# Kernel tuning notes

Measured on AMD Instinct MI355X. Metric: run time of the kernel, lower is better.

The kernel has to match this reference:

```python
import jax, jax.numpy as jnp
import numpy as np

IN_FEATURES = 4096
OUT_FEATURES = 11008
B, S = 4, 2048


def setup_inputs() -> dict:
    key = jax.random.key(0)
    k1, k2, k3, k4 = jax.random.split(key, 4)
    x = jax.random.normal(k1, (B, S, IN_FEATURES), dtype=jnp.float32)
    # int8 quantized weights in [-127, 127]
    weight_quantized = jax.random.randint(k2, (OUT_FEATURES, IN_FEATURES), -127, 128, dtype=jnp.int8)
    # realistic per-channel scales (positive, small)
    weight_scale = jax.random.uniform(k3, (OUT_FEATURES,), dtype=jnp.float32, minval=1e-4, maxval=2e-2)
    bias = jax.random.normal(k4, (OUT_FEATURES,), dtype=jnp.float32) * 0.01
    return {"x": x, "weight_quantized": weight_quantized, "weight_scale": weight_scale, "bias": bias}


def reference(x, weight_quantized, weight_scale, bias):
    # Dequantize: W = int8.float() * scale[:, None]  (symmetric, per-channel)
    w = weight_quantized.astype(jnp.float32) * weight_scale[:, None]  # [out, in]
    # F.linear: y = x @ W^T + b
    return jnp.einsum('bsi,oi->bso', x, w) + bias
```

## Files before the change

### kernel.cpp

```cpp
#include <hip/hip_runtime.h>
#include <hip/hip_bf16.h>
#include <stdint.h>


#define M_TOTAL 8192
#define K_TOTAL 4096
#define N_TOTAL 11008
#define NT 32
#define NBM 64
#define NBN 86

typedef __attribute__((ext_vector_type(4))) int int4v;


__global__ __launch_bounds__(256) void quant_x_kernel(const float* __restrict__ x,
                                                      signed char* __restrict__ xq,
                                                      float* __restrict__ sx) {
    const int row = blockIdx.x;
    const int tid = threadIdx.x;
    const float* xr = x + (size_t)row * K_TOTAL + tid * 16;

    float4 v0 = reinterpret_cast<const float4*>(xr)[0];
    float4 v1 = reinterpret_cast<const float4*>(xr)[1];
    float4 v2 = reinterpret_cast<const float4*>(xr)[2];
    float4 v3 = reinterpret_cast<const float4*>(xr)[3];

    float m = 0.f;
    m = fmaxf(m, fmaxf(fmaxf(fabsf(v0.x), fabsf(v0.y)), fmaxf(fabsf(v0.z), fabsf(v0.w))));
    m = fmaxf(m, fmaxf(fmaxf(fabsf(v1.x), fabsf(v1.y)), fmaxf(fabsf(v1.z), fabsf(v1.w))));
    m = fmaxf(m, fmaxf(fmaxf(fabsf(v2.x), fabsf(v2.y)), fmaxf(fabsf(v2.z), fabsf(v2.w))));
    m = fmaxf(m, fmaxf(fmaxf(fabsf(v3.x), fabsf(v3.y)), fmaxf(fabsf(v3.z), fabsf(v3.w))));

    for (int d = 1; d < 64; d <<= 1) m = fmaxf(m, __shfl_xor(m, d));
    __shared__ float wm_[4];
    if ((tid & 63) == 0) wm_[tid >> 6] = m;
    __syncthreads();
    m = fmaxf(fmaxf(wm_[0], wm_[1]), fmaxf(wm_[2], wm_[3]));

    const float inv = (m > 0.f) ? (127.f / m) : 0.f;
    if (tid == 0) sx[row] = (m > 0.f) ? (m / 127.f) : 0.f;

    float tmp[16] = {v0.x,v0.y,v0.z,v0.w, v1.x,v1.y,v1.z,v1.w,
                     v2.x,v2.y,v2.z,v2.w, v3.x,v3.y,v3.z,v3.w};
    int q[16];
#pragma unroll
    for (int i = 0; i < 16; ++i) {
        int t = __float2int_rn(tmp[i] * inv);
        q[i] = t > 127 ? 127 : (t < -127 ? -127 : t);
    }
    int4v o;
#pragma unroll
    for (int w = 0; w < 4; ++w)
        o[w] = (q[w*4] & 255) | ((q[w*4+1] & 255) << 8) |
               ((q[w*4+2] & 255) << 16) | ((q[w*4+3] & 255) << 24);
    *reinterpret_cast<int4v*>(xq + (size_t)row * K_TOTAL + tid * 16) = o;
}


__global__ __launch_bounds__(256) void cvt_w_kernel(const int* __restrict__ in,
                                                    signed char* __restrict__ out, int nitems) {
    bool is8 = false;
    for (int i = 0; i < 256; ++i) {
        int v = in[i];
        if (v < -127 || v > 127) { is8 = true; break; }
    }
    int stride = gridDim.x * blockDim.x;
    if (!is8) {
        for (int i = blockIdx.x * blockDim.x + threadIdx.x; i < nitems; i += stride) {
            const int* p = in + (size_t)i * 16;
            int4v o;
#pragma unroll
            for (int w = 0; w < 4; ++w)
                o[w] = (p[w*4] & 255) | ((p[w*4+1] & 255) << 8) |
                       ((p[w*4+2] & 255) << 16) | ((p[w*4+3] & 255) << 24);
            *reinterpret_cast<int4v*>(out + (size_t)i * 16) = o;
        }
    } else {
        const int4v* in16 = reinterpret_cast<const int4v*>(in);
        for (int i = blockIdx.x * blockDim.x + threadIdx.x; i < nitems; i += stride)
            *reinterpret_cast<int4v*>(out + (size_t)i * 16) = in16[i];
    }
}


#define GLOAD16(g, l) __builtin_amdgcn_global_load_lds( \
    (const __attribute__((address_space(1))) void*)(g), \
    (__attribute__((address_space(3))) void*)(l), 16, 0, 0)


#define RD_A(dst, base, KX)                                                     \
    _Pragma("unroll")                                                           \
    for (int i_ = 0; i_ < 4; ++i_)                                              \
        dst[i_] = *(const int4v*)((base) + (wm * 64 + i_ * 16 + fr) * 128 + (KX));
#define RD_B(dst, base, KX)                                                     \
    _Pragma("unroll")                                                           \
    for (int n_ = 0; n_ < 4; ++n_)                                              \
        dst[n_] = *(const int4v*)((base) + 16384 + (wn * 64 + n_ * 16 + fr) * 128 + (KX));
#define MFMA16(fa, fb)                                                          \
    __builtin_amdgcn_s_setprio(1);                                              \
    _Pragma("unroll")                                                           \
    for (int i_ = 0; i_ < 4; ++i_) {                                            \
        _Pragma("unroll")                                                       \
        for (int n_ = 0; n_ < 4; ++n_)                                          \
            acc[i_][n_] = __builtin_amdgcn_mfma_i32_16x16x64_i8(                \
                fa[i_], fb[n_], acc[i_][n_], 0, 0, 0);                          \
    }                                                                           \
    __builtin_amdgcn_s_setprio(0);
#define STAGE_A(asrc, buf)                                                      \
    _Pragma("unroll")                                                           \
    for (int i_ = 0; i_ < 4; ++i_)                                              \
        GLOAD16((asrc) + soff[i_], (buf) + (c0 + i_) * 1024);
#define STAGE_B(bsrc, buf)                                                      \
    _Pragma("unroll")                                                           \
    for (int i_ = 0; i_ < 4; ++i_)                                              \
        GLOAD16((bsrc) + soff[i_], (buf) + 16384 + (c0 + i_) * 1024);

__global__ __launch_bounds__(256, 2) void gemm_kernel(const unsigned char* __restrict__ A,
                                                      const unsigned char* __restrict__ B,
                                                      const float* __restrict__ sx,
                                                      const float* __restrict__ scale,
                                                      const float* __restrict__ bias,
                                                      float* __restrict__ C) {
    __shared__ unsigned char sh[65536];

    const int tid  = threadIdx.x;
    const int wv   = tid >> 6;
    const int lane = tid & 63;
    const int wm   = wv >> 1;
    const int wn   = wv & 1;

    const int xcd = blockIdx.x & 7;
    const int l   = blockIdx.x >> 3;
    const int band = l / 344;
    const int lb   = l - band * 344;
    const int st   = lb >> 4;
    const int r    = lb & 15;
    int bm_l, bn;
    if (st < 21) { bm_l = band * 4 + (r >> 2); bn = st * 4 + (r & 3); }
    else         { bm_l = band * 4 + (r >> 1); bn = 84 + (r & 1); }
    const int bm = xcd * 8 + bm_l;

    const int fr  = lane & 15;
    const int fq  = lane >> 4;
    const int swz = fr & 7;
    const int kx0 = (fq ^ swz) * 16;
    const int kx1 = ((4 + fq) ^ swz) * 16;

    const int c0 = wv * 4;
    const int rl = lane >> 3;
    const int sg = (lane & 7) ^ rl;
    size_t soff[4];
#pragma unroll
    for (int i = 0; i < 4; ++i)
        soff[i] = (size_t)((c0 + i) * 8 + rl) * K_TOTAL + sg * 16;

    const unsigned char* aS = A + (size_t)bm * 128 * K_TOTAL;
    const unsigned char* bS = B + (size_t)bn * 128 * K_TOTAL;
    unsigned char* buf0 = sh;
    unsigned char* buf1 = sh + 32768;

    int4v acc[4][4] = {};
    int4v afX[4], afY[4], bf0v[4], bf1v[4];

    STAGE_A(aS, buf0)
    STAGE_B(bS, buf0)
    STAGE_B(bS + 128, buf1)
    asm volatile("s_waitcnt vmcnt(4)" ::: "memory");
    __builtin_amdgcn_s_barrier();
    RD_A(afX, buf0, kx0)
    RD_B(bf0v, buf0, kx0)
    RD_B(bf1v, buf0, kx1)

#pragma unroll 1
    for (int t = 0; t < NT; ++t) {
        const int p = t & 1;
        unsigned char* bp = p ? buf1 : buf0;
        unsigned char* bq = p ? buf0 : buf1;

        RD_A(afY, bp, kx1)
        if (t + 1 < NT) { STAGE_A(aS + (size_t)(t + 1) * 128, bq) }
        MFMA16(afX, bf0v)
        asm volatile("s_waitcnt lgkmcnt(0)" ::: "memory");
        __builtin_amdgcn_s_barrier();

        if (t + 2 < NT) { STAGE_B(bS + (size_t)(t + 2) * 128, bp) }
        MFMA16(afY, bf1v)
        if (t + 1 < NT) {
            if (t + 2 < NT) { asm volatile("s_waitcnt vmcnt(4)" ::: "memory"); }
            else            { asm volatile("s_waitcnt vmcnt(0)" ::: "memory"); }
        }
        __builtin_amdgcn_s_barrier();
        if (t + 1 < NT) {
            RD_A(afX, bq, kx0)
            RD_B(bf0v, bq, kx0)
            RD_B(bf1v, bq, kx1)
        }
    }

    const int crow0 = bm * 128 + wm * 64;
    const int ccol0 = bn * 128 + wn * 64;
    float scv[4], bsv[4];
#pragma unroll
    for (int n = 0; n < 4; ++n) {
        const int col = ccol0 + n * 16 + fr;
        scv[n] = scale[col];
        bsv[n] = bias[col];
    }
#pragma unroll
    for (int fm = 0; fm < 4; ++fm) {
#pragma unroll
        for (int j = 0; j < 4; ++j) {
            const int row = crow0 + fm * 16 + fq * 4 + j;
            const float sr = sx[row];
            float* cp = C + (size_t)row * N_TOTAL + ccol0 + fr;
#pragma unroll
            for (int n = 0; n < 4; ++n)
                cp[n * 16] = (float)acc[fm][n][j] * (sr * scv[n]) + bsv[n];
        }
    }
}


__global__ __launch_bounds__(256) void gemm_fallback(const float* __restrict__ x,
                                                     const int* __restrict__ w,
                                                     const float* __restrict__ scale,
                                                     const float* __restrict__ bias,
                                                     float* __restrict__ C) {
    bool is8 = false;
    for (int i = 0; i < 256; ++i) {
        int v = w[i];
        if (v < -127 || v > 127) { is8 = true; break; }
    }
    const signed char* w8 = (const signed char*)w;

    __shared__ float As[64][16];
    __shared__ float Bs[64][16];
    const int nbn = N_TOTAL / 64;
    const int bm = blockIdx.x / nbn;
    const int bn = blockIdx.x % nbn;
    const int tid = threadIdx.x;
    const int tx = tid & 15, ty = tid >> 4;

    float acc[4][4] = {};
    for (int kt = 0; kt < K_TOTAL; kt += 16) {
        for (int i = 0; i < 4; ++i) {
            int idx = tid + i * 256;
            int rr = idx >> 4, cc = idx & 15;
            As[rr][cc] = x[(size_t)(bm * 64 + rr) * K_TOTAL + kt + cc];
            size_t widx = (size_t)(bn * 64 + rr) * K_TOTAL + kt + cc;
            Bs[rr][cc] = is8 ? (float)w8[widx] : (float)w[widx];
        }
        __syncthreads();
        for (int kk = 0; kk < 16; ++kk) {
            float a[4], b[4];
            for (int i = 0; i < 4; ++i) a[i] = As[ty * 4 + i][kk];
            for (int j = 0; j < 4; ++j) b[j] = Bs[tx * 4 + j][kk];
            for (int i = 0; i < 4; ++i)
                for (int j = 0; j < 4; ++j) acc[i][j] += a[i] * b[j];
        }
        __syncthreads();
    }
    for (int j = 0; j < 4; ++j) {
        int col = bn * 64 + tx * 4 + j;
        float s = scale[col], bb = bias[col];
        for (int i = 0; i < 4; ++i) {
            int row = bm * 64 + ty * 4 + i;
            C[(size_t)row * N_TOTAL + col] = acc[i][j] * s + bb;
        }
    }
}


extern "C" void kernel_launch(void* const* d_in, const int* in_sizes, int n_in,
                              void* d_out, int out_size, void* d_ws, size_t ws_size,
                              hipStream_t stream) {
    const float* x     = (const float*)d_in[0];
    const int*   wq    = (const int*)d_in[1];
    const float* scale = (const float*)d_in[2];
    const float* bias  = (const float*)d_in[3];
    float*       out   = (float*)d_out;

    const size_t x_bytes = (size_t)M_TOTAL * K_TOTAL;
    const size_t w_bytes = (size_t)N_TOTAL * K_TOTAL;
    const size_t need = x_bytes + w_bytes + M_TOTAL * sizeof(float);

    if (ws_size >= need) {
        signed char* xq = (signed char*)d_ws;
        signed char* wb = (signed char*)d_ws + x_bytes;
        float*       sx = (float*)((char*)d_ws + x_bytes + w_bytes);

        quant_x_kernel<<<M_TOTAL, 256, 0, stream>>>(x, xq, sx);
        cvt_w_kernel<<<2048, 256, 0, stream>>>(wq, wb, (int)(w_bytes / 16));
        dim3 grid(NBM * NBN);
        gemm_kernel<<<grid, 256, 0, stream>>>((const unsigned char*)xq,
                                              (const unsigned char*)wb,
                                              sx, scale, bias, out);
    } else {
        dim3 grid((M_TOTAL / 64) * (N_TOTAL / 64));
        gemm_fallback<<<grid, 256, 0, stream>>>(x, wq, scale, bias, out);
    }
}
```

Before: 471.9 us.

## Enlarge int8 GEMM block tile to 256x256 with 512 threads

Grows the GEMM macro tile from 128x128 to 256x256 and doubles the block to 8 waves in a 2x4 layout, each wave computing a 128x64 sub-tile. The double-buffered LDS staging grows to 128 KB, and the block-to-tile mapping is simplified to 4 row tiles per XCD. The aim is to roughly halve global and LDS traffic per MFMA through more operand reuse. In exchange, each thread needs far more registers (128 accumulator values plus larger fragments) under a launch bound of 2 blocks of 512 threads, so spilling is likely. The 128 KB LDS footprint also limits each CU to one block, and 1376 tiles over the CUs leave a tail.

```diff
diff --git a/kernel.cpp b/kernel.cpp
--- a/kernel.cpp
+++ b/kernel.cpp
@@ -7,8 +7,8 @@
 #define K_TOTAL 4096
 #define N_TOTAL 11008
 #define NT 32
-#define NBM 64
-#define NBN 86
+#define NBM 32
+#define NBN 43
 
 typedef __attribute__((ext_vector_type(4))) int int4v;
 
@@ -88,18 +88,18 @@
     (__attribute__((address_space(3))) void*)(l), 16, 0, 0)
 
 
-#define RD_A(dst, base, KX)                                                     \
-    _Pragma("unroll")                                                           \
-    for (int i_ = 0; i_ < 4; ++i_)                                              \
-        dst[i_] = *(const int4v*)((base) + (wm * 64 + i_ * 16 + fr) * 128 + (KX));
-#define RD_B(dst, base, KX)                                                     \
+#define RD_A8(dst, base, KX)                                                    \
+    _Pragma("unroll")                                                           \
+    for (int i_ = 0; i_ < 8; ++i_)                                              \
+        dst[i_] = *(const int4v*)((base) + (wm * 128 + i_ * 16 + fr) * 128 + (KX));
+#define RD_B4(dst, base, KX)                                                    \
     _Pragma("unroll")                                                           \
     for (int n_ = 0; n_ < 4; ++n_)                                              \
-        dst[n_] = *(const int4v*)((base) + 16384 + (wn * 64 + n_ * 16 + fr) * 128 + (KX));
-#define MFMA16(fa, fb)                                                          \
+        dst[n_] = *(const int4v*)((base) + 32768 + (wn * 64 + n_ * 16 + fr) * 128 + (KX));
+#define MFMA32(fa, fb)                                                          \
     __builtin_amdgcn_s_setprio(1);                                              \
     _Pragma("unroll")                                                           \
-    for (int i_ = 0; i_ < 4; ++i_) {                                            \
+    for (int i_ = 0; i_ < 8; ++i_) {                                            \
         _Pragma("unroll")                                                       \
         for (int n_ = 0; n_ < 4; ++n_)                                          \
             acc[i_][n_] = __builtin_amdgcn_mfma_i32_16x16x64_i8(                \
@@ -113,32 +113,26 @@
 #define STAGE_B(bsrc, buf)                                                      \
     _Pragma("unroll")                                                           \
     for (int i_ = 0; i_ < 4; ++i_)                                              \
-        GLOAD16((bsrc) + soff[i_], (buf) + 16384 + (c0 + i_) * 1024);
-
-__global__ __launch_bounds__(256, 2) void gemm_kernel(const unsigned char* __restrict__ A,
+        GLOAD16((bsrc) + soff[i_], (buf) + 32768 + (c0 + i_) * 1024);
+
+__global__ __launch_bounds__(512, 2) void gemm_kernel(const unsigned char* __restrict__ A,
                                                       const unsigned char* __restrict__ B,
                                                       const float* __restrict__ sx,
                                                       const float* __restrict__ scale,
                                                       const float* __restrict__ bias,
                                                       float* __restrict__ C) {
-    __shared__ unsigned char sh[65536];
+    __shared__ unsigned char sh[131072];
 
     const int tid  = threadIdx.x;
     const int wv   = tid >> 6;
     const int lane = tid & 63;
-    const int wm   = wv >> 1;
-    const int wn   = wv & 1;
+    const int wm   = wv >> 2;
+    const int wn   = wv & 3;
 
     const int xcd = blockIdx.x & 7;
     const int l   = blockIdx.x >> 3;
-    const int band = l / 344;
-    const int lb   = l - band * 344;
-    const int st   = lb >> 4;
-    const int r    = lb & 15;
-    int bm_l, bn;
-    if (st < 21) { bm_l = band * 4 + (r >> 2); bn = st * 4 + (r & 3); }
-    else         { bm_l = band * 4 + (r >> 1); bn = 84 + (r & 1); }
-    const int bm = xcd * 8 + bm_l;
+    const int bm  = xcd * 4 + (l & 3);
+    const int bn  = l >> 2;
 
     const int fr  = lane & 15;
     const int fq  = lane >> 4;
@@ -149,27 +143,27 @@
     const int c0 = wv * 4;
     const int rl = lane >> 3;
     const int sg = (lane & 7) ^ rl;
-    size_t soff[4];
+    int soff[4];
 #pragma unroll
     for (int i = 0; i < 4; ++i)
-        soff[i] = (size_t)((c0 + i) * 8 + rl) * K_TOTAL + sg * 16;
-
-    const unsigned char* aS = A + (size_t)bm * 128 * K_TOTAL;
-    const unsigned char* bS = B + (size_t)bn * 128 * K_TOTAL;
+        soff[i] = ((c0 + i) * 8 + rl) * K_TOTAL + sg * 16;
+
+    const unsigned char* aS = A + (size_t)bm * 256 * K_TOTAL;
+    const unsigned char* bS = B + (size_t)bn * 256 * K_TOTAL;
     unsigned char* buf0 = sh;
-    unsigned char* buf1 = sh + 32768;
-
-    int4v acc[4][4] = {};
-    int4v afX[4], afY[4], bf0v[4], bf1v[4];
+    unsigned char* buf1 = sh + 65536;
+
+    int4v acc[8][4] = {};
+    int4v afX[8], afY[8], bf0v[4], bf1v[4];
 
     STAGE_A(aS, buf0)
     STAGE_B(bS, buf0)
     STAGE_B(bS + 128, buf1)
     asm volatile("s_waitcnt vmcnt(4)" ::: "memory");
     __builtin_amdgcn_s_barrier();
-    RD_A(afX, buf0, kx0)
-    RD_B(bf0v, buf0, kx0)
-    RD_B(bf1v, buf0, kx1)
+    RD_A8(afX, buf0, kx0)
+    RD_B4(bf0v, buf0, kx0)
+    RD_B4(bf1v, buf0, kx1)
 
 #pragma unroll 1
     for (int t = 0; t < NT; ++t) {
@@ -177,28 +171,28 @@
         unsigned char* bp = p ? buf1 : buf0;
         unsigned char* bq = p ? buf0 : buf1;
 
-        RD_A(afY, bp, kx1)
+        RD_A8(afY, bp, kx1)
         if (t + 1 < NT) { STAGE_A(aS + (size_t)(t + 1) * 128, bq) }
-        MFMA16(afX, bf0v)
+        MFMA32(afX, bf0v)
         asm volatile("s_waitcnt lgkmcnt(0)" ::: "memory");
         __builtin_amdgcn_s_barrier();
 
         if (t + 2 < NT) { STAGE_B(bS + (size_t)(t + 2) * 128, bp) }
-        MFMA16(afY, bf1v)
+        MFMA32(afY, bf1v)
         if (t + 1 < NT) {
             if (t + 2 < NT) { asm volatile("s_waitcnt vmcnt(4)" ::: "memory"); }
             else            { asm volatile("s_waitcnt vmcnt(0)" ::: "memory"); }
         }
         __builtin_amdgcn_s_barrier();
         if (t + 1 < NT) {
-            RD_A(afX, bq, kx0)
-            RD_B(bf0v, bq, kx0)
-            RD_B(bf1v, bq, kx1)
-        }
-    }
-
-    const int crow0 = bm * 128 + wm * 64;
-    const int ccol0 = bn * 128 + wn * 64;
+            RD_A8(afX, bq, kx0)
+            RD_B4(bf0v, bq, kx0)
+            RD_B4(bf1v, bq, kx1)
+        }
+    }
+
+    const int crow0 = bm * 256 + wm * 128;
+    const int ccol0 = bn * 256 + wn * 64;
     float scv[4], bsv[4];
 #pragma unroll
     for (int n = 0; n < 4; ++n) {
@@ -207,7 +201,7 @@
         bsv[n] = bias[col];
     }
 #pragma unroll
-    for (int fm = 0; fm < 4; ++fm) {
+    for (int fm = 0; fm < 8; ++fm) {
 #pragma unroll
         for (int j = 0; j < 4; ++j) {
             const int row = crow0 + fm * 16 + fq * 4 + j;
@@ -292,7 +286,7 @@
         quant_x_kernel<<<M_TOTAL, 256, 0, stream>>>(x, xq, sx);
         cvt_w_kernel<<<2048, 256, 0, stream>>>(wq, wb, (int)(w_bytes / 16));
         dim3 grid(NBM * NBN);
-        gemm_kernel<<<grid, 256, 0, stream>>>((const unsigned char*)xq,
+        gemm_kernel<<<grid, 512, 0, stream>>>((const unsigned char*)xq,
                                               (const unsigned char*)wb,
                                               sx, scale, bias, out);
     } else {
```

After: 462.5 us. 1.02x faster.
